# Kernel optimization log

Hardware: AMD Instinct MI355X
Metric: run time of the kernel (lower is better)

## Reference

```python
import math
import jax, jax.numpy as jnp
import numpy as np

CROP_H = 28  # self.height
OUT_HW = 224  # final F.interpolate size


def _thetas_and_widths(boxes_np, H, W):
    """Host-side replication of cv2.minAreaRect/getAffineTransform + param2theta.
    boxes_np: [N,1,4] int (x1,y1,x3,y3). Returns thetas [N,2,3] f32, widths [N] int."""
    thetas, widths = [], []
    for b in boxes_np:
        x1, y1, x3, y3 = [float(v) for v in b[0]]
        bw, bh = abs(x3 - x1), abs(y3 - y1)
        box_w, box_h = max(bw, bh), min(bw, bh)  # minAreaRect + swap so box_w >= box_h
        wb = min(math.ceil(CROP_H * box_w / box_h), W)
        # cv2.getAffineTransform: affine maps (x1,y1)->(0,0), (x3,y1)->(wb,0), (x1,y3)->(0,CROP_H)
        src = np.array([[x1, y1, 1.0], [x3, y1, 1.0], [x1, y3, 1.0]], dtype=np.float64)
        dst = np.array([[0.0, 0.0], [wb, 0.0], [0.0, CROP_H]], dtype=np.float64)
        P = np.linalg.solve(src, dst)           # src @ P = dst -> affine = P.T (2x3)
        A = np.vstack([P.T, [0.0, 0.0, 1.0]])   # homogeneous 3x3
        Ai = np.linalg.inv(A)                    # param2theta inverts the affine
        th = np.zeros((2, 3), dtype=np.float64)
        th[0, 0] = Ai[0, 0]
        th[0, 1] = Ai[0, 1] * H / W
        th[0, 2] = Ai[0, 2] * 2.0 / W + th[0, 0] + th[0, 1] - 1.0
        th[1, 0] = Ai[1, 0] * W / H
        th[1, 1] = Ai[1, 1]
        th[1, 2] = Ai[1, 2] * 2.0 / H + th[1, 0] + th[1, 1] - 1.0
        thetas.append(th)
        widths.append(wb)
    return np.stack(thetas).astype(np.float32), np.array(widths, dtype=np.int64)


def _interp_matrix(out_size, in_size):
    """Row-stochastic linear-interpolation matrix, bilinear align_corners=True."""
    pos = jnp.linspace(0.0, in_size - 1.0, out_size)
    i0 = jnp.clip(jnp.floor(pos), 0, in_size - 2).astype(jnp.int32)
    t = pos - i0.astype(pos.dtype)
    r = jnp.arange(out_size)
    M = jnp.zeros((out_size, in_size), jnp.float32)
    return M.at[r, i0].add(1.0 - t).at[r, i0 + 1].add(t)


def _forward(feature, boxes, num_boxes):
    C, H, W = feature.shape[1], feature.shape[2], feature.shape[3]
    boxes_np = np.asarray(boxes)
    thetas_np, widths = _thetas_and_widths(boxes_np, H, W)
    thetas = jnp.asarray(thetas_np)                              # [N,2,3]

    # F.affine_grid(theta, (N,C,H,W), align_corners=True)
    xs = jnp.linspace(-1.0, 1.0, W)
    ys = jnp.linspace(-1.0, 1.0, H)
    gx0, gy0 = jnp.meshgrid(xs, ys, indexing='xy')               # [H,W]
    base = jnp.stack([gx0, gy0, jnp.ones_like(gx0)], axis=-1)    # [H,W,3]
    grid = jnp.einsum('nij,hwj->nhwi', thetas, base)             # [N,H,W,2] (x,y)

    # F.grid_sample bilinear, padding_mode='zeros', align_corners=True
    feat0 = feature[0]                                           # [C,H,W]
    ix = (grid[..., 0] + 1.0) * (W - 1) * 0.5                    # [N,H,W]
    iy = (grid[..., 1] + 1.0) * (H - 1) * 0.5
    x0f, y0f = jnp.floor(ix), jnp.floor(iy)
    x0, y0 = x0f.astype(jnp.int32), y0f.astype(jnp.int32)
    wx, wy = ix - x0f, iy - y0f

    def g(xi, yi):
        valid = (xi >= 0) & (xi < W) & (yi >= 0) & (yi < H)
        v = feat0[:, jnp.clip(yi, 0, H - 1), jnp.clip(xi, 0, W - 1)]  # [C,N,H,W]
        return v * valid[None].astype(feat0.dtype)

    rot = (((1 - wx) * (1 - wy))[None] * g(x0, y0)
           + (wx * (1 - wy))[None] * g(x0 + 1, y0)
           + ((1 - wx) * wy)[None] * g(x0, y0 + 1)
           + (wx * wy)[None] * g(x0 + 1, y0 + 1))                 # [C,N,H,W]
    rot = jnp.transpose(rot, (1, 0, 2, 3))                        # [N,C,H,W]

    # crop [:, :, :28, :w_i] and zero-pad to max width (mask == crop+pad)
    maxw = int(widths.max())
    mask = (jnp.arange(maxw)[None, :] < jnp.asarray(widths)[:, None]).astype(rot.dtype)
    cropped = rot[:, :, :CROP_H, :maxw] * mask[:, None, None, :]  # [N,C,28,maxw]

    # sort by width descending (np.argsort then reversed, as in the original)
    order = np.argsort(widths)[::-1].copy()
    cropped = cropped[jnp.asarray(order)]

    # F.interpolate to (224,224), bilinear, align_corners=True (separable)
    My = _interp_matrix(OUT_HW, CROP_H)                           # [224,28]
    Mx = _interp_matrix(OUT_HW, maxw)                             # [224,maxw]
    return jnp.einsum('nchw,ph,qw->ncpq', cropped, My, Mx)


def setup_inputs() -> dict:
    key = jax.random.key(0)
    N, C, H, W = 32, 32, 256, 256
    feature = jax.random.normal(key, (1, C, H, W), dtype=jnp.float32)
    rng = np.random.default_rng(0)
    x1 = rng.integers(0, 170, N)
    y1 = rng.integers(0, 200, N)
    bw = rng.integers(20, 80, N)
    bh = rng.integers(8, 48, N)
    x3 = np.minimum(x1 + bw, W - 1)
    y3 = np.minimum(y1 + bh, H - 1)
    boxes = jnp.asarray(np.stack([x1, y1, x3, y3], axis=1)[:, None, :].astype(np.int64))
    return {"feature": feature, "boxes": boxes, "num_boxes": N}


def reference(feature, boxes, num_boxes):
    return _forward(feature, boxes, num_boxes)
```

## Files before the change

### kernel.cpp

```cpp
#include <hip/hip_runtime.h>

#define NBOX   32
#define NCH    32
#define IMG    256
#define CROPH  28
#define OUTHW  224
#define TSTR   257

__device__ __forceinline__ void xss_stage(long long* k, int* a,
                                          const int* p, int mask) {
  long long nk[8]; int na[8];
  for (int j = 0; j < 8; ++j) {
    long long kb = k[p[j]]; int ab = a[p[j]];
    long long mn = (kb < k[j]) ? kb : k[j];
    long long mx = (kb < k[j]) ? k[j] : kb;
    long long sel = ((mask >> j) & 1) ? mx : mn;
    na[j] = (sel == k[j]) ? a[j] : ab;
    nk[j] = sel;
  }
  for (int j = 0; j < 8; ++j) { k[j] = nk[j]; a[j] = na[j]; }
}
__device__ __forceinline__ void xss_rev(long long* k, int* a) {
  for (int j = 0; j < 4; ++j) {
    long long tk = k[j]; k[j] = k[7-j]; k[7-j] = tk;
    int ta = a[j]; a[j] = a[7-j]; a[7-j] = ta;
  }
}
__device__ __forceinline__ void xss_coex(long long* k1, int* a1,
                                         long long* k2, int* a2) {
  for (int j = 0; j < 8; ++j) {
    long long ka = k1[j], kb = k2[j];
    int aa = a1[j], ab = a2[j];
    bool alem = (ka <= kb);
    k1[j] = alem ? ka : kb;  a1[j] = alem ? aa : ab;
    k2[j] = alem ? kb : ka;  a2[j] = alem ? ab : aa;
  }
}
__device__ __forceinline__ void xss_sort8(long long* k, int* a) {
  const int P1[8] = {1,0,3,2,5,4,7,6};
  const int P2[8] = {2,3,0,1,6,7,4,5};
  const int P3[8] = {3,2,1,0,7,6,5,4};
  const int P7[8] = {7,6,5,4,3,2,1,0};
  xss_stage(k, a, P1, 0xAA);
  xss_stage(k, a, P3, 0xCC);
  xss_stage(k, a, P1, 0xAA);
  xss_stage(k, a, P7, 0xF0);
  xss_stage(k, a, P2, 0xCC);
  xss_stage(k, a, P1, 0xAA);
}
__device__ __forceinline__ void xss_merge8(long long* k, int* a) {
  const int P1[8] = {1,0,3,2,5,4,7,6};
  const int P2[8] = {2,3,0,1,6,7,4,5};
  const int P4[8] = {4,5,6,7,0,1,2,3};
  xss_stage(k, a, P4, 0xF0);
  xss_stage(k, a, P2, 0xCC);
  xss_stage(k, a, P1, 0xAA);
}
__device__ __forceinline__ void xss_merge_pair(long long* kA, int* aA,
                                               long long* kB, int* aB) {
  xss_rev(kB, aB);
  xss_coex(kA, aA, kB, aB);
  xss_rev(kB, aB);
  xss_merge8(kA, aA);
  xss_merge8(kB, aB);
}

__global__ void prep_kernel(const int* __restrict__ boxes_raw,
                            int* __restrict__ wsi, float* __restrict__ th) {
  __shared__ int    s_w[NBOX];
  __shared__ double s_t[NBOX][4];
  __shared__ int    s_asc[NBOX];
  __shared__ int    s_i64;
  int lane = threadIdx.x;

  if (lane == 0) {
    int i64 = 1;
    for (int i = 1; i < NBOX*4; i += 2)
      if (boxes_raw[i] != 0) { i64 = 0; break; }
    s_i64 = i64;
  }
  __syncthreads();
  bool i64mode = (s_i64 != 0);

  if (lane < NBOX) {
    int x1, y1, x3, y3;
    if (i64mode) {
      x1 = boxes_raw[(lane*4+0)*2]; y1 = boxes_raw[(lane*4+1)*2];
      x3 = boxes_raw[(lane*4+2)*2]; y3 = boxes_raw[(lane*4+3)*2];
    } else {
      x1 = boxes_raw[lane*4+0]; y1 = boxes_raw[lane*4+1];
      x3 = boxes_raw[lane*4+2]; y3 = boxes_raw[lane*4+3];
    }
    int bw = x3 > x1 ? x3-x1 : x1-x3;
    int bh = y3 > y1 ? y3-y1 : y1-y3;
    int bmax = bw > bh ? bw : bh;
    int bmin = bw > bh ? bh : bw;
    if (bmin < 1) bmin = 1;
    int wb = (CROPH*bmax + bmin - 1) / bmin;
    if (wb > IMG) wb = IMG;
    s_w[lane] = wb;
    double a = (double)(x3-x1) / (double)wb;
    double e = (double)(y3-y1) / (double)CROPH;
    s_t[lane][0] = a;
    s_t[lane][1] = (double)x1 * (2.0/(double)IMG) + a - 1.0;
    s_t[lane][2] = e;
    s_t[lane][3] = (double)y1 * (2.0/(double)IMG) + e - 1.0;
  }
  __syncthreads();

  if (lane == 0) {
    long long K[4][8]; int A[4][8];
    for (int v = 0; v < 4; ++v)
      for (int j = 0; j < 8; ++j) {
        A[v][j] = 8*v + j;
        K[v][j] = (long long)s_w[8*v + j];
      }
    for (int v = 0; v < 4; ++v) xss_sort8(K[v], A[v]);
    xss_merge_pair(K[0], A[0], K[1], A[1]);
    xss_merge_pair(K[2], A[2], K[3], A[3]);
    xss_rev(K[3], A[3]); xss_coex(K[0], A[0], K[3], A[3]); xss_rev(K[3], A[3]);
    xss_rev(K[2], A[2]); xss_coex(K[1], A[1], K[2], A[2]); xss_rev(K[2], A[2]);
    xss_coex(K[0], A[0], K[1], A[1]);
    xss_coex(K[2], A[2], K[3], A[3]);
    for (int v = 0; v < 4; ++v) xss_merge8(K[v], A[v]);
    for (int v = 0; v < 4; ++v)
      for (int j = 0; j < 8; ++j) s_asc[8*v + j] = A[v][j];
    int maxw = 0;
    for (int i = 0; i < NBOX; ++i) if (s_w[i] > maxw) maxw = s_w[i];
    wsi[0] = maxw;
  }
  __syncthreads();

  if (lane < NBOX) {
    int src = s_asc[NBOX-1-lane];
    wsi[1+lane]   = s_w[src];
    th[lane*4+0]  = (float)s_t[src][0];
    th[lane*4+1]  = (float)s_t[src][1];
    th[lane*4+2]  = (float)s_t[src][2];
    th[lane*4+3]  = (float)s_t[src][3];
  }
}

__global__ __launch_bounds__(256)
void fused_kernel(const float* __restrict__ feat,
                  const int* __restrict__ wsi,
                  const float* __restrict__ th,
                  float* __restrict__ out) {
  __shared__ float tile[CROPH][TSTR];
  int c = blockIdx.x, n = blockIdx.y;
  int tid = threadIdx.x;

  int maxw  = wsi[0];
  int width = wsi[1+n];
  float t00 = th[n*4+0], t02 = th[n*4+1], t11 = th[n*4+2], t12 = th[n*4+3];

  const float* fc = feat + c*IMG*IMG;
  int w = tid;
  if (w < width) {
    float gx = -1.f + (2.f/255.f)*(float)w;
    float ix = (t00*gx + t02 + 1.f)*127.5f;
    float xf = floorf(ix);
    int   x0 = (int)xf;
    x0 = min(max(x0, 0), IMG-2);
    float wx = ix - xf;
    const float* col = fc + x0;
    for (int h = 0; h < CROPH; ++h) {
      float gy = -1.f + (2.f/255.f)*(float)h;
      float iy = (t11*gy + t12 + 1.f)*127.5f;
      float yf = floorf(iy);
      int   y0 = (int)yf;
      y0 = min(max(y0, 0), IMG-2);
      float wy = iy - yf;
      const float* r0 = col + y0*IMG;
      float a0 = r0[0],   a1 = r0[1];
      float b0 = r0[IMG], b1 = r0[IMG+1];
      float ta = a0 + wx*(a1-a0);
      float tb = b0 + wx*(b1-b0);
      tile[h][w] = ta + wy*(tb-ta);
    }
  } else {
    for (int h = 0; h < CROPH; ++h) tile[h][w] = 0.f;
  }
  __syncthreads();

  int wave = tid >> 6;
  int lane = tid & 63;
  if (lane < OUTHW/4) {
    int qb = lane * 4;
    const float xs = (float)(maxw-1)/(float)(OUTHW-1);
    float tx[4]; int xi[4];
#pragma unroll
    for (int j = 0; j < 4; ++j) {
      float qx = (float)(qb+j) * xs;
      float xf = floorf(qx);
      int x = (int)xf; if (x > maxw-2) x = maxw-2;
      xi[j] = x; tx[j] = qx - (float)x;
    }
    const float pys = (float)(CROPH-1)/(float)(OUTHW-1);
    float* op = out + ((size_t)(n*NCH + c))*OUTHW*OUTHW + qb;

    int cur = -2;
    float vtop[4], vbot[4];
    for (int p = wave; p < OUTHW; p += 4) {
      float py = (float)p * pys;
      int h0 = (int)py; if (h0 > CROPH-2) h0 = CROPH-2;
      float ty = py - (float)h0;
      if (h0 != cur) {
        if (h0 == cur+1) {
#pragma unroll
          for (int j = 0; j < 4; ++j) vtop[j] = vbot[j];
        } else {
#pragma unroll
          for (int j = 0; j < 4; ++j) {
            float a0 = tile[h0][xi[j]], a1 = tile[h0][xi[j]+1];
            vtop[j] = a0 + tx[j]*(a1-a0);
          }
        }
#pragma unroll
        for (int j = 0; j < 4; ++j) {
          float b0 = tile[h0+1][xi[j]], b1 = tile[h0+1][xi[j]+1];
          vbot[j] = b0 + tx[j]*(b1-b0);
        }
        cur = h0;
      }
      float4 o;
      o.x = vtop[0] + ty*(vbot[0]-vtop[0]);
      o.y = vtop[1] + ty*(vbot[1]-vtop[1]);
      o.z = vtop[2] + ty*(vbot[2]-vtop[2]);
      o.w = vtop[3] + ty*(vbot[3]-vtop[3]);
      *(float4*)(op + (size_t)p*OUTHW) = o;
    }
  }
}

extern "C" void kernel_launch(void* const* d_in, const int* in_sizes, int n_in,
                              void* d_out, int out_size, void* d_ws, size_t ws_size,
                              hipStream_t stream) {
  const float* feat  = (const float*)d_in[0];
  const int*   boxes = (const int*)d_in[1];
  float* out = (float*)d_out;

  int*   wsi = (int*)d_ws;
  float* th  = (float*)((char*)d_ws + 512);

  prep_kernel<<<1, 64, 0, stream>>>(boxes, wsi, th);
  fused_kernel<<<dim3(NCH, NBOX), 256, 0, stream>>>(feat, wsi, th, out);
}
```

Before: 220.8 us.

## Fuse box preprocessing into main kernel and use nontemporal output stores

Removes the separate single-block prep kernel: every block now recomputes box widths, the sort and its own theta in shared memory, which drops one launch and the workspace round trip. The int64 check now uses a wavefront ballot instead of a serial loop. Output writes switch to nontemporal stores to avoid polluting the cache with the large write-only result. The cost is redundant serial sort work in thread 0 of all 1024 blocks, which delays the main compute in each block.

```diff
diff --git a/kernel.cpp b/kernel.cpp
--- a/kernel.cpp
+++ b/kernel.cpp
@@ -6,6 +6,8 @@
 #define CROPH  28
 #define OUTHW  224
 #define TSTR   257
+
+typedef float f4 __attribute__((ext_vector_type(4)));
 
 __device__ __forceinline__ void xss_stage(long long* k, int* a,
                                           const int* p, int mask) {
@@ -65,31 +67,34 @@
   xss_merge8(kB, aB);
 }
 
-__global__ void prep_kernel(const int* __restrict__ boxes_raw,
-                            int* __restrict__ wsi, float* __restrict__ th) {
-  __shared__ int    s_w[NBOX];
-  __shared__ double s_t[NBOX][4];
-  __shared__ int    s_asc[NBOX];
-  __shared__ int    s_i64;
-  int lane = threadIdx.x;
-
-  if (lane == 0) {
-    int i64 = 1;
-    for (int i = 1; i < NBOX*4; i += 2)
-      if (boxes_raw[i] != 0) { i64 = 0; break; }
-    s_i64 = i64;
+__global__ __launch_bounds__(256)
+void fused_all(const float* __restrict__ feat,
+               const int* __restrict__ boxes_raw,
+               float* __restrict__ out) {
+  __shared__ float tile[CROPH][TSTR];
+  __shared__ int   s_w[NBOX];
+  __shared__ int   s_i64, s_maxw, s_wd;
+  __shared__ float s_th[4];
+
+  int c = blockIdx.x, n = blockIdx.y;
+  int tid = threadIdx.x;
+
+  if (tid < 64) {
+    int v = boxes_raw[2*tid + 1];
+    unsigned long long b = __ballot(v != 0);
+    if (tid == 0) s_i64 = (b == 0ULL) ? 1 : 0;
   }
   __syncthreads();
   bool i64mode = (s_i64 != 0);
 
-  if (lane < NBOX) {
+  if (tid < NBOX) {
     int x1, y1, x3, y3;
     if (i64mode) {
-      x1 = boxes_raw[(lane*4+0)*2]; y1 = boxes_raw[(lane*4+1)*2];
-      x3 = boxes_raw[(lane*4+2)*2]; y3 = boxes_raw[(lane*4+3)*2];
+      x1 = boxes_raw[(tid*4+0)*2]; y1 = boxes_raw[(tid*4+1)*2];
+      x3 = boxes_raw[(tid*4+2)*2]; y3 = boxes_raw[(tid*4+3)*2];
     } else {
-      x1 = boxes_raw[lane*4+0]; y1 = boxes_raw[lane*4+1];
-      x3 = boxes_raw[lane*4+2]; y3 = boxes_raw[lane*4+3];
+      x1 = boxes_raw[tid*4+0]; y1 = boxes_raw[tid*4+1];
+      x3 = boxes_raw[tid*4+2]; y3 = boxes_raw[tid*4+3];
     }
     int bw = x3 > x1 ? x3-x1 : x1-x3;
     int bh = y3 > y1 ? y3-y1 : y1-y3;
@@ -98,17 +103,11 @@
     if (bmin < 1) bmin = 1;
     int wb = (CROPH*bmax + bmin - 1) / bmin;
     if (wb > IMG) wb = IMG;
-    s_w[lane] = wb;
-    double a = (double)(x3-x1) / (double)wb;
-    double e = (double)(y3-y1) / (double)CROPH;
-    s_t[lane][0] = a;
-    s_t[lane][1] = (double)x1 * (2.0/(double)IMG) + a - 1.0;
-    s_t[lane][2] = e;
-    s_t[lane][3] = (double)y1 * (2.0/(double)IMG) + e - 1.0;
-  }
-  __syncthreads();
-
-  if (lane == 0) {
+    s_w[tid] = wb;
+  }
+  __syncthreads();
+
+  if (tid == 0) {
     long long K[4][8]; int A[4][8];
     for (int v = 0; v < 4; ++v)
       for (int j = 0; j < 8; ++j) {
@@ -123,38 +122,37 @@
     xss_coex(K[0], A[0], K[1], A[1]);
     xss_coex(K[2], A[2], K[3], A[3]);
     for (int v = 0; v < 4; ++v) xss_merge8(K[v], A[v]);
-    for (int v = 0; v < 4; ++v)
-      for (int j = 0; j < 8; ++j) s_asc[8*v + j] = A[v][j];
+
+    int flat = NBOX-1-n;
+    int src = A[flat >> 3][flat & 7];
+
     int maxw = 0;
     for (int i = 0; i < NBOX; ++i) if (s_w[i] > maxw) maxw = s_w[i];
-    wsi[0] = maxw;
-  }
-  __syncthreads();
-
-  if (lane < NBOX) {
-    int src = s_asc[NBOX-1-lane];
-    wsi[1+lane]   = s_w[src];
-    th[lane*4+0]  = (float)s_t[src][0];
-    th[lane*4+1]  = (float)s_t[src][1];
-    th[lane*4+2]  = (float)s_t[src][2];
-    th[lane*4+3]  = (float)s_t[src][3];
-  }
-}
-
-__global__ __launch_bounds__(256)
-void fused_kernel(const float* __restrict__ feat,
-                  const int* __restrict__ wsi,
-                  const float* __restrict__ th,
-                  float* __restrict__ out) {
-  __shared__ float tile[CROPH][TSTR];
-  int c = blockIdx.x, n = blockIdx.y;
-  int tid = threadIdx.x;
-
-  int maxw  = wsi[0];
-  int width = wsi[1+n];
-  float t00 = th[n*4+0], t02 = th[n*4+1], t11 = th[n*4+2], t12 = th[n*4+3];
-
-  const float* fc = feat + c*IMG*IMG;
+    s_maxw = maxw;
+    s_wd   = s_w[src];
+
+    int x1, y1, x3, y3;
+    if (i64mode) {
+      x1 = boxes_raw[(src*4+0)*2]; y1 = boxes_raw[(src*4+1)*2];
+      x3 = boxes_raw[(src*4+2)*2]; y3 = boxes_raw[(src*4+3)*2];
+    } else {
+      x1 = boxes_raw[src*4+0]; y1 = boxes_raw[src*4+1];
+      x3 = boxes_raw[src*4+2]; y3 = boxes_raw[src*4+3];
+    }
+    double a = (double)(x3-x1) / (double)s_w[src];
+    double e = (double)(y3-y1) / (double)CROPH;
+    s_th[0] = (float)a;
+    s_th[1] = (float)((double)x1 * (2.0/(double)IMG) + a - 1.0);
+    s_th[2] = (float)e;
+    s_th[3] = (float)((double)y1 * (2.0/(double)IMG) + e - 1.0);
+  }
+  __syncthreads();
+
+  int maxw  = s_maxw;
+  int width = s_wd;
+  float t00 = s_th[0], t02 = s_th[1], t11 = s_th[2], t12 = s_th[3];
+
+  const float* fc = feat + (size_t)c*IMG*IMG;
   int w = tid;
   if (w < width) {
     float gx = -1.f + (2.f/255.f)*(float)w;
@@ -223,12 +221,12 @@
         }
         cur = h0;
       }
-      float4 o;
+      f4 o;
       o.x = vtop[0] + ty*(vbot[0]-vtop[0]);
       o.y = vtop[1] + ty*(vbot[1]-vtop[1]);
       o.z = vtop[2] + ty*(vbot[2]-vtop[2]);
       o.w = vtop[3] + ty*(vbot[3]-vtop[3]);
-      *(float4*)(op + (size_t)p*OUTHW) = o;
+      __builtin_nontemporal_store(o, (f4*)(op + (size_t)p*OUTHW));
     }
   }
 }
@@ -239,10 +237,7 @@
   const float* feat  = (const float*)d_in[0];
   const int*   boxes = (const int*)d_in[1];
   float* out = (float*)d_out;
-
-  int*   wsi = (int*)d_ws;
-  float* th  = (float*)((char*)d_ws + 512);
-
-  prep_kernel<<<1, 64, 0, stream>>>(boxes, wsi, th);
-  fused_kernel<<<dim3(NCH, NBOX), 256, 0, stream>>>(feat, wsi, th, out);
-}
+  (void)d_ws; (void)ws_size;
+
+  fused_all<<<dim3(NCH, NBOX), 256, 0, stream>>>(feat, boxes, out);
+}
```

Result: slower. 251.1 us (+13.7%).
